# Optimization experiments

Measured on AMD Instinct MI355X. Metric: run time of the kernel, lower is better.

Reference implementation:

```python
import jax, jax.numpy as jnp
import numpy as np

N_NODES = 65536
N_EDGES = 1048576
DIM = 64
N_GRAPHS = 16


def setup_inputs() -> dict:
    key = jax.random.key(0)
    ks = jax.random.split(key, 8)
    node_feats = jax.random.normal(ks[0], (N_NODES, DIM), dtype=jnp.float32)
    edge_index = jax.random.randint(ks[1], (2, N_EDGES), 0, N_NODES, dtype=jnp.int32)
    batch_num_nodes = jnp.full((N_GRAPHS,), N_NODES // N_GRAPHS, dtype=jnp.int32)
    s = 1.0 / np.sqrt(DIM)
    W1 = jax.random.normal(ks[2], (DIM, DIM), dtype=jnp.float32) * s
    W2 = jax.random.normal(ks[3], (DIM, DIM), dtype=jnp.float32) * s
    W3 = jax.random.normal(ks[4], (DIM, DIM), dtype=jnp.float32) * s
    b1 = jnp.zeros((DIM,), jnp.float32)
    b2 = jnp.zeros((DIM,), jnp.float32)
    b3 = jnp.zeros((DIM,), jnp.float32)
    return {"node_feats": node_feats, "edge_index": edge_index,
            "batch_num_nodes": batch_num_nodes,
            "W1": W1, "b1": b1, "W2": W2, "b2": b2, "W3": W3, "b3": b3}


def _graph_conv(x, src, dst, W, b, n_nodes):
    # DGL GraphConv with norm='both': D_out^{-1/2} A^T D_in^{-1/2} style sym norm
    ones = jnp.ones((src.shape[0],), x.dtype)
    deg_out = jnp.clip(jax.ops.segment_sum(ones, src, num_segments=n_nodes), 1.0)
    deg_in = jnp.clip(jax.ops.segment_sum(ones, dst, num_segments=n_nodes), 1.0)
    h = x * jax.lax.rsqrt(deg_out)[:, None]          # [N, d] scale by src out-deg
    agg = jax.ops.segment_sum(h[src], dst, num_segments=n_nodes)  # gather+scatter
    agg = agg * jax.lax.rsqrt(deg_in)[:, None]
    return agg @ W + b


def _unbatch(h, batch_num_nodes):
    # pad each graph's node block to max_num_node -> [B, max_n, d]
    bnn = np.asarray(batch_num_nodes)
    B = bnn.shape[0]
    max_n = int(bnn.max())
    offsets = np.concatenate([[0], np.cumsum(bnn)])
    graph_id = np.repeat(np.arange(B), bnn)                 # [N_total]
    pos = np.arange(int(offsets[-1])) - offsets[graph_id]   # position within graph
    out = jnp.zeros((B, max_n, h.shape[1]), h.dtype)
    return out.at[jnp.asarray(graph_id), jnp.asarray(pos)].set(h)


def reference(node_feats, edge_index, batch_num_nodes, W1, b1, W2, b2, W3, b3):
    src, dst = edge_index[0], edge_index[1]
    n = node_feats.shape[0]
    h = jax.nn.relu(_graph_conv(node_feats, src, dst, W1, b1, n))
    h = jax.nn.relu(_graph_conv(h, src, dst, W2, b2, n))
    h = _graph_conv(h, src, dst, W3, b3, n)
    return _unbatch(h, batch_num_nodes)
```

## Files before the change

### kernel.cpp

```cpp
#include <hip/hip_runtime.h>
#include <hip/hip_fp16.h>


#define N_NODES 65536
#define N_EDGES 1048576
#define DIM 64

#define CHUNKS 256
#define EPC (N_EDGES / CHUNKS)
#define HB 128
#define OH_WORDS 16384

struct alignas(8) h4 { __half2 a, b; };

__global__ void edge_hist(const int* __restrict__ src, const int* __restrict__ dst,
                          int* __restrict__ block_hist, unsigned* __restrict__ partial,
                          uint2* __restrict__ zeroA, uint2* __restrict__ zeroB) {
    __shared__ unsigned h[OH_WORDS];
    __shared__ int bh[2][256];
    int t = threadIdx.x;
    int j = blockIdx.x;
    for (int i = t; i < OH_WORDS; i += 256) h[i] = 0;
    bh[0][t] = 0; bh[1][t] = 0;
    __syncthreads();
    if (j == 0) {
        if (t < 16) zeroA[t] = make_uint2(0u, 0u);
        else if (t < 32) zeroB[t - 16] = make_uint2(0u, 0u);
    }
    int base = j * (2 * EPC);
    for (int i = t; i < 2 * EPC; i += 256) {
        int s = src[base + i];
        int d = dst[base + i];
        atomicAdd(&h[s >> 2], 1u << ((s & 3) * 8));
        atomicAdd(&bh[i >> 12][d >> 8], 1);
    }
    __syncthreads();
    unsigned* dp = partial + (size_t)j * OH_WORDS;
    for (int i = t; i < OH_WORDS; i += 256) dp[i] = h[i];
    block_hist[t * CHUNKS + 2 * j]     = bh[0][t];
    block_hist[t * CHUNKS + 2 * j + 1] = bh[1][t];
}

__global__ void part_scan(const int* __restrict__ bh, int* __restrict__ so) {
    __shared__ int s[1024];
    int t = threadIdx.x;
    const int4* b4 = (const int4*)(bh + t * 64);
    int4 v[16];
    int sum = 0;
    #pragma unroll
    for (int i = 0; i < 16; i++) {
        v[i] = b4[i];
        sum += v[i].x + v[i].y + v[i].z + v[i].w;
    }
    s[t] = sum;
    __syncthreads();
    for (int off = 1; off < 1024; off <<= 1) {
        int u = (t >= off) ? s[t - off] : 0;
        __syncthreads();
        s[t] += u;
        __syncthreads();
    }
    int run = s[t] - sum;
    int* o = so + t * 64;
    #pragma unroll
    for (int i = 0; i < 16; i++) {
        o[4 * i + 0] = run; run += v[i].x;
        o[4 * i + 1] = run; run += v[i].y;
        o[4 * i + 2] = run; run += v[i].z;
        o[4 * i + 3] = run; run += v[i].w;
    }
}

__global__ void part_scatter(const int* __restrict__ src, const int* __restrict__ dst,
                             const int* __restrict__ so, int* __restrict__ bpack) {
    __shared__ int hist[256], sc[256], off[256], cur[256], gbase[256];
    __shared__ int sorted[EPC];
    __shared__ unsigned char pos2b[EPC];
    int t = threadIdx.x;
    int j = blockIdx.x;
    hist[t] = 0;
    gbase[t] = so[t * CHUNKS + j];
    __syncthreads();
    int base = j * EPC;
    int sv[16], dv[16];
    #pragma unroll
    for (int u = 0; u < 16; u++) {
        int i = base + u * 256 + t;
        sv[u] = src[i];
        dv[u] = dst[i];
        atomicAdd(&hist[dv[u] >> 8], 1);
    }
    __syncthreads();
    int hv = hist[t];
    sc[t] = hv;
    __syncthreads();
    for (int o = 1; o < 256; o <<= 1) {
        int u = (t >= o) ? sc[t - o] : 0;
        __syncthreads();
        sc[t] += u;
        __syncthreads();
    }
    int myoff = sc[t] - hv;
    off[t] = myoff;
    cur[t] = myoff;
    __syncthreads();
    for (int p = myoff, e = myoff + hv; p < e; p++)
        pos2b[p] = (unsigned char)t;
    #pragma unroll
    for (int u = 0; u < 16; u++) {
        int b = dv[u] >> 8;
        int r = atomicAdd(&cur[b], 1);
        sorted[r] = sv[u] | ((dv[u] & 255) << 16);
    }
    __syncthreads();
    #pragma unroll
    for (int u = 0; u < 16; u++) {
        int i = u * 256 + t;
        int b = pos2b[i];
        bpack[gbase[b] + (i - off[b])] = sorted[i];
    }
}

__global__ void bucket_fused(const int* __restrict__ bpack, const int* __restrict__ so,
                             int* __restrict__ row_start, float* __restrict__ rs_in,
                             unsigned short* __restrict__ csr_src) {
    __shared__ int stage[8192];
    __shared__ unsigned short sorted[8192];
    __shared__ int h[256], sc[256], cur[256];
    int b = blockIdx.x;
    int t = threadIdx.x;
    int beg = so[b * CHUNKS];
    int end = (b == 255) ? N_EDGES : so[(b + 1) * CHUNKS];
    int n = end - beg;
    h[t] = 0;
    __syncthreads();
    for (int i = t; i < n; i += 256) {
        int p = bpack[beg + i];
        if (i < 8192) stage[i] = p;
        atomicAdd(&h[(p >> 16) & 255], 1);
    }
    __syncthreads();
    int d = h[t];
    sc[t] = d;
    __syncthreads();
    for (int off = 1; off < 256; off <<= 1) {
        int v = (t >= off) ? sc[t - off] : 0;
        __syncthreads();
        sc[t] += v;
        __syncthreads();
    }
    int excl = sc[t] - d;
    int node = b * 256 + t;
    row_start[node] = beg + excl;
    rs_in[node] = rsqrtf(d < 1 ? 1.0f : (float)d);
    if (node == N_NODES - 1) row_start[N_NODES] = N_EDGES;
    cur[t] = excl;
    __syncthreads();
    if (n <= 8192) {
        for (int i = t; i < n; i += 256) {
            int p = stage[i];
            int r = atomicAdd(&cur[(p >> 16) & 255], 1);
            sorted[r] = (unsigned short)(p & 0xFFFF);
        }
        __syncthreads();
        for (int i = t; i < n; i += 256)
            csr_src[beg + i] = sorted[i];
    } else {
        cur[t] = beg + excl;
        __syncthreads();
        for (int i = t; i < n; i += 256) {
            int p = (i < 8192) ? stage[i] : bpack[beg + i];
            int pos = atomicAdd(&cur[(p >> 16) & 255], 1);
            csr_src[pos] = (unsigned short)(p & 0xFFFF);
        }
    }
}

__global__ void oh2p_prescale(const unsigned* __restrict__ partial,
                              float* __restrict__ rs_out,
                              const float4* __restrict__ x4, h4* __restrict__ xs) {
    __shared__ int4 psum[256];
    __shared__ float rsl[256];
    int b = blockIdx.x;
    int t = threadIdx.x;
    {
        int wl = t & 63;
        int q  = t >> 6;
        int w = b * 64 + wl;
        int c0 = 0, c1 = 0, c2 = 0, c3 = 0;
        const unsigned* p = partial + (size_t)(q * (HB / 4)) * OH_WORDS + w;
        #pragma unroll 4
        for (int c = 0; c < HB / 4; c++) {
            unsigned v = p[(size_t)c * OH_WORDS];
            c0 += (int)(v & 255u);
            c1 += (int)((v >> 8) & 255u);
            c2 += (int)((v >> 16) & 255u);
            c3 += (int)(v >> 24);
        }
        psum[t] = make_int4(c0, c1, c2, c3);
    }
    __syncthreads();
    if (t < 64) {
        int4 a = psum[t], b2 = psum[t + 64], c = psum[t + 128], d = psum[t + 192];
        int c0 = a.x + b2.x + c.x + d.x;
        int c1 = a.y + b2.y + c.y + d.y;
        int c2 = a.z + b2.z + c.z + d.z;
        int c3 = a.w + b2.w + c.w + d.w;
        int w = b * 64 + t;
        float4 r = make_float4(rsqrtf(c0 < 1 ? 1.0f : (float)c0),
                               rsqrtf(c1 < 1 ? 1.0f : (float)c1),
                               rsqrtf(c2 < 1 ? 1.0f : (float)c2),
                               rsqrtf(c3 < 1 ? 1.0f : (float)c3));
        ((float4*)rs_out)[w] = r;
        rsl[t * 4 + 0] = r.x; rsl[t * 4 + 1] = r.y;
        rsl[t * 4 + 2] = r.z; rsl[t * 4 + 3] = r.w;
    }
    __syncthreads();
    int rowbase = b * 4096;
    for (int i = t; i < 4096; i += 256) {
        float r = rsl[i >> 4];
        float4 v = x4[rowbase + i];
        h4 o;
        o.a = __float22half2_rn(make_float2(v.x * r, v.y * r));
        o.b = __float22half2_rn(make_float2(v.z * r, v.w * r));
        xs[rowbase + i] = o;
    }
}

template<bool SCALE_OUT>
__global__ void fused_layer(const uint4* __restrict__ xs16, const int* __restrict__ row_start,
                            const unsigned short* __restrict__ csr,
                            const float* __restrict__ rs_out, const float* __restrict__ rs_in,
                            const float* __restrict__ W, const float* __restrict__ b,
                            void* __restrict__ outp) {
    __shared__ float4 Ws4[DIM * 16];
    __shared__ float4 bs4[16];
    {
        const float4* Wg = (const float4*)W;
        for (int i = threadIdx.x; i < DIM * 16; i += blockDim.x) Ws4[i] = Wg[i];
        if (threadIdx.x < 16) bs4[threadIdx.x] = ((const float4*)b)[threadIdx.x];
    }
    __syncthreads();

    int wave_id = threadIdx.x >> 6;
    int lane = threadIdx.x & 63;
    int g = lane >> 3;
    int l = lane & 7;
    int node = blockIdx.x * 32 + wave_id * 8 + g;

    int beg = row_start[node];
    int end = row_start[node + 1];

    float a0 = 0.f, a1 = 0.f, a2 = 0.f, a3 = 0.f,
          a4 = 0.f, a5 = 0.f, a6 = 0.f, a7 = 0.f;
    for (int k = beg; k < end; k += 16) {
        int s[16];
        #pragma unroll
        for (int j = 0; j < 16; j++) {
            int kk = k + j;
            int idx = csr[kk];
            s[j] = (kk < end) ? idx : N_NODES;
        }
        uint4 v[16];
        #pragma unroll
        for (int j = 0; j < 16; j++) v[j] = xs16[s[j] * 8 + l];
        #pragma unroll
        for (int j = 0; j < 16; j++) {
            float2 f0 = __half22float2(*(const __half2*)&v[j].x);
            float2 f1 = __half22float2(*(const __half2*)&v[j].y);
            float2 f2 = __half22float2(*(const __half2*)&v[j].z);
            float2 f3 = __half22float2(*(const __half2*)&v[j].w);
            a0 += f0.x; a1 += f0.y; a2 += f1.x; a3 += f1.y;
            a4 += f2.x; a5 += f2.y; a6 += f3.x; a7 += f3.y;
        }
    }
    float ri = rs_in[node];
    a0 *= ri; a1 *= ri; a2 *= ri; a3 *= ri;
    a4 *= ri; a5 *= ri; a6 *= ri; a7 *= ri;

    float4 o0 = bs4[2 * l];
    float4 o1 = bs4[2 * l + 1];
    int gbase = g << 3;
    #pragma unroll
    for (int m = 0; m < 8; m++) {
        float q0 = __shfl(a0, gbase + m, 64);
        float q1 = __shfl(a1, gbase + m, 64);
        float q2 = __shfl(a2, gbase + m, 64);
        float q3 = __shfl(a3, gbase + m, 64);
        float q4 = __shfl(a4, gbase + m, 64);
        float q5 = __shfl(a5, gbase + m, 64);
        float q6 = __shfl(a6, gbase + m, 64);
        float q7 = __shfl(a7, gbase + m, 64);
        int rb = (8 * m) * 16 + 2 * l;
        float4 w;
        w = Ws4[rb];            o0.x += q0*w.x; o0.y += q0*w.y; o0.z += q0*w.z; o0.w += q0*w.w;
        w = Ws4[rb + 1];        o1.x += q0*w.x; o1.y += q0*w.y; o1.z += q0*w.z; o1.w += q0*w.w;
        w = Ws4[rb + 16];       o0.x += q1*w.x; o0.y += q1*w.y; o0.z += q1*w.z; o0.w += q1*w.w;
        w = Ws4[rb + 17];       o1.x += q1*w.x; o1.y += q1*w.y; o1.z += q1*w.z; o1.w += q1*w.w;
        w = Ws4[rb + 32];       o0.x += q2*w.x; o0.y += q2*w.y; o0.z += q2*w.z; o0.w += q2*w.w;
        w = Ws4[rb + 33];       o1.x += q2*w.x; o1.y += q2*w.y; o1.z += q2*w.z; o1.w += q2*w.w;
        w = Ws4[rb + 48];       o0.x += q3*w.x; o0.y += q3*w.y; o0.z += q3*w.z; o0.w += q3*w.w;
        w = Ws4[rb + 49];       o1.x += q3*w.x; o1.y += q3*w.y; o1.z += q3*w.z; o1.w += q3*w.w;
        w = Ws4[rb + 64];       o0.x += q4*w.x; o0.y += q4*w.y; o0.z += q4*w.z; o0.w += q4*w.w;
        w = Ws4[rb + 65];       o1.x += q4*w.x; o1.y += q4*w.y; o1.z += q4*w.z; o1.w += q4*w.w;
        w = Ws4[rb + 80];       o0.x += q5*w.x; o0.y += q5*w.y; o0.z += q5*w.z; o0.w += q5*w.w;
        w = Ws4[rb + 81];       o1.x += q5*w.x; o1.y += q5*w.y; o1.z += q5*w.z; o1.w += q5*w.w;
        w = Ws4[rb + 96];       o0.x += q6*w.x; o0.y += q6*w.y; o0.z += q6*w.z; o0.w += q6*w.w;
        w = Ws4[rb + 97];       o1.x += q6*w.x; o1.y += q6*w.y; o1.z += q6*w.z; o1.w += q6*w.w;
        w = Ws4[rb + 112];      o0.x += q7*w.x; o0.y += q7*w.y; o0.z += q7*w.z; o0.w += q7*w.w;
        w = Ws4[rb + 113];      o1.x += q7*w.x; o1.y += q7*w.y; o1.z += q7*w.z; o1.w += q7*w.w;
    }
    if (SCALE_OUT) {
        float ro = rs_out[node];
        o0.x = (o0.x < 0.f ? 0.f : o0.x) * ro;
        o0.y = (o0.y < 0.f ? 0.f : o0.y) * ro;
        o0.z = (o0.z < 0.f ? 0.f : o0.z) * ro;
        o0.w = (o0.w < 0.f ? 0.f : o0.w) * ro;
        o1.x = (o1.x < 0.f ? 0.f : o1.x) * ro;
        o1.y = (o1.y < 0.f ? 0.f : o1.y) * ro;
        o1.z = (o1.z < 0.f ? 0.f : o1.z) * ro;
        o1.w = (o1.w < 0.f ? 0.f : o1.w) * ro;
        uint4 ho;
        *(__half2*)&ho.x = __float22half2_rn(make_float2(o0.x, o0.y));
        *(__half2*)&ho.y = __float22half2_rn(make_float2(o0.z, o0.w));
        *(__half2*)&ho.z = __float22half2_rn(make_float2(o1.x, o1.y));
        *(__half2*)&ho.w = __float22half2_rn(make_float2(o1.z, o1.w));
        ((uint4*)outp)[node * 8 + l] = ho;
    } else {
        float4* o4 = (float4*)outp;
        o4[node * 16 + 2 * l]     = o0;
        o4[node * 16 + 2 * l + 1] = o1;
    }
}

extern "C" void kernel_launch(void* const* d_in, const int* in_sizes, int n_in,
                              void* d_out, int out_size, void* d_ws, size_t ws_size,
                              hipStream_t stream) {
    const float* x   = (const float*)d_in[0];
    const int*   ei  = (const int*)d_in[1];
    const int*   src = ei;
    const int*   dst = ei + N_EDGES;
    const float* W1 = (const float*)d_in[3];
    const float* b1 = (const float*)d_in[4];
    const float* W2 = (const float*)d_in[5];
    const float* b2 = (const float*)d_in[6];
    const float* W3 = (const float*)d_in[7];
    const float* b3 = (const float*)d_in[8];
    float* out = (float*)d_out;

    char* ws = (char*)d_ws;
    float* rs        = (float*)ws;
    float* rs_out    = rs;
    float* rs_in     = rs + N_NODES;
    int*   row_start = (int*)(rs + 2 * N_NODES);
    int*   block_h   = row_start + (N_NODES + 256);
    int*   so        = block_h + 256 * CHUNKS;
    unsigned short* csr_src = (unsigned short*)(so + 256 * CHUNKS);
    h4*    bufA      = (h4*)(csr_src + N_EDGES + 16);
    h4*    bufB      = bufA + (size_t)(N_NODES + 1) * 16;
    unsigned* partial = (unsigned*)(bufB + (size_t)(N_NODES + 1) * 16);
    int*   bpack     = (int*)bufB;
    uint2* zeroA     = (uint2*)(bufA + (size_t)N_NODES * 16);
    uint2* zeroB     = (uint2*)(bufB + (size_t)N_NODES * 16);

    const int fb = N_NODES / 32;

    edge_hist    <<<HB, 256, 0, stream>>>(src, dst, block_h, partial, zeroA, zeroB);
    part_scan    <<<1, 1024, 0, stream>>>(block_h, so);
    part_scatter <<<CHUNKS, 256, 0, stream>>>(src, dst, so, bpack);
    bucket_fused <<<256, 256, 0, stream>>>(bpack, so, row_start, rs_in, csr_src);
    oh2p_prescale<<<256, 256, 0, stream>>>(partial, rs_out, (const float4*)x, bufA);

    fused_layer<true ><<<fb, 256, 0, stream>>>((const uint4*)bufA, row_start, csr_src, rs_out, rs_in, W1, b1, (void*)bufB);
    fused_layer<true ><<<fb, 256, 0, stream>>>((const uint4*)bufB, row_start, csr_src, rs_out, rs_in, W2, b2, (void*)bufA);
    fused_layer<false><<<fb, 256, 0, stream>>>((const uint4*)bufA, row_start, csr_src, rs_out, rs_in, W3, b3, (void*)out);
}
```

Before: 236.6 us.

## Fuse CSR preprocessing kernels into one cooperative kernel with grid syncs

Merges the five preprocessing kernels (edge histogram, partition scan, scatter, bucket sort, prescale) into a single cooperative kernel of 256 blocks separated by grid.sync barriers. The single-block 1024-thread scan becomes a two-level parallel scan: each block scans one row of block histograms, then scans the row totals. The goal is to remove kernel launch gaps and the serial single-block scan. In exchange, the large 67KB shared buffer per block may limit occupancy, and half the blocks sit idle during the histogram phase.

Measured after the change: 358.8 us. +51.6%, slower.

```diff
diff --git a/kernel.cpp b/kernel.cpp
--- a/kernel.cpp
+++ b/kernel.cpp
@@ -1,5 +1,8 @@
 #include <hip/hip_runtime.h>
 #include <hip/hip_fp16.h>
+#include <hip/hip_cooperative_groups.h>
+
+namespace cg = cooperative_groups;
 
 
 #define N_NODES 65536
@@ -13,177 +16,64 @@
 
 struct alignas(8) h4 { __half2 a, b; };
 
-__global__ void edge_hist(const int* __restrict__ src, const int* __restrict__ dst,
-                          int* __restrict__ block_hist, unsigned* __restrict__ partial,
-                          uint2* __restrict__ zeroA, uint2* __restrict__ zeroB) {
-    __shared__ unsigned h[OH_WORDS];
-    __shared__ int bh[2][256];
-    int t = threadIdx.x;
-    int j = blockIdx.x;
-    for (int i = t; i < OH_WORDS; i += 256) h[i] = 0;
-    bh[0][t] = 0; bh[1][t] = 0;
-    __syncthreads();
-    if (j == 0) {
-        if (t < 16) zeroA[t] = make_uint2(0u, 0u);
-        else if (t < 32) zeroB[t - 16] = make_uint2(0u, 0u);
-    }
-    int base = j * (2 * EPC);
-    for (int i = t; i < 2 * EPC; i += 256) {
-        int s = src[base + i];
-        int d = dst[base + i];
-        atomicAdd(&h[s >> 2], 1u << ((s & 3) * 8));
-        atomicAdd(&bh[i >> 12][d >> 8], 1);
-    }
-    __syncthreads();
-    unsigned* dp = partial + (size_t)j * OH_WORDS;
-    for (int i = t; i < OH_WORDS; i += 256) dp[i] = h[i];
-    block_hist[t * CHUNKS + 2 * j]     = bh[0][t];
-    block_hist[t * CHUNKS + 2 * j + 1] = bh[1][t];
-}
-
-__global__ void part_scan(const int* __restrict__ bh, int* __restrict__ so) {
-    __shared__ int s[1024];
-    int t = threadIdx.x;
-    const int4* b4 = (const int4*)(bh + t * 64);
-    int4 v[16];
-    int sum = 0;
-    #pragma unroll
-    for (int i = 0; i < 16; i++) {
-        v[i] = b4[i];
-        sum += v[i].x + v[i].y + v[i].z + v[i].w;
-    }
-    s[t] = sum;
-    __syncthreads();
-    for (int off = 1; off < 1024; off <<= 1) {
-        int u = (t >= off) ? s[t - off] : 0;
-        __syncthreads();
-        s[t] += u;
-        __syncthreads();
-    }
-    int run = s[t] - sum;
-    int* o = so + t * 64;
-    #pragma unroll
-    for (int i = 0; i < 16; i++) {
-        o[4 * i + 0] = run; run += v[i].x;
-        o[4 * i + 1] = run; run += v[i].y;
-        o[4 * i + 2] = run; run += v[i].z;
-        o[4 * i + 3] = run; run += v[i].w;
-    }
-}
-
-__global__ void part_scatter(const int* __restrict__ src, const int* __restrict__ dst,
-                             const int* __restrict__ so, int* __restrict__ bpack) {
-    __shared__ int hist[256], sc[256], off[256], cur[256], gbase[256];
-    __shared__ int sorted[EPC];
-    __shared__ unsigned char pos2b[EPC];
-    int t = threadIdx.x;
-    int j = blockIdx.x;
-    hist[t] = 0;
-    gbase[t] = so[t * CHUNKS + j];
-    __syncthreads();
-    int base = j * EPC;
-    int sv[16], dv[16];
-    #pragma unroll
-    for (int u = 0; u < 16; u++) {
-        int i = base + u * 256 + t;
-        sv[u] = src[i];
-        dv[u] = dst[i];
-        atomicAdd(&hist[dv[u] >> 8], 1);
-    }
-    __syncthreads();
-    int hv = hist[t];
-    sc[t] = hv;
-    __syncthreads();
-    for (int o = 1; o < 256; o <<= 1) {
-        int u = (t >= o) ? sc[t - o] : 0;
-        __syncthreads();
-        sc[t] += u;
-        __syncthreads();
-    }
-    int myoff = sc[t] - hv;
-    off[t] = myoff;
-    cur[t] = myoff;
-    __syncthreads();
-    for (int p = myoff, e = myoff + hv; p < e; p++)
-        pos2b[p] = (unsigned char)t;
-    #pragma unroll
-    for (int u = 0; u < 16; u++) {
-        int b = dv[u] >> 8;
-        int r = atomicAdd(&cur[b], 1);
-        sorted[r] = sv[u] | ((dv[u] & 255) << 16);
-    }
-    __syncthreads();
-    #pragma unroll
-    for (int u = 0; u < 16; u++) {
-        int i = u * 256 + t;
-        int b = pos2b[i];
-        bpack[gbase[b] + (i - off[b])] = sorted[i];
-    }
-}
-
-__global__ void bucket_fused(const int* __restrict__ bpack, const int* __restrict__ so,
-                             int* __restrict__ row_start, float* __restrict__ rs_in,
-                             unsigned short* __restrict__ csr_src) {
-    __shared__ int stage[8192];
-    __shared__ unsigned short sorted[8192];
-    __shared__ int h[256], sc[256], cur[256];
-    int b = blockIdx.x;
-    int t = threadIdx.x;
-    int beg = so[b * CHUNKS];
-    int end = (b == 255) ? N_EDGES : so[(b + 1) * CHUNKS];
-    int n = end - beg;
-    h[t] = 0;
-    __syncthreads();
-    for (int i = t; i < n; i += 256) {
-        int p = bpack[beg + i];
-        if (i < 8192) stage[i] = p;
-        atomicAdd(&h[(p >> 16) & 255], 1);
-    }
-    __syncthreads();
-    int d = h[t];
-    sc[t] = d;
-    __syncthreads();
-    for (int off = 1; off < 256; off <<= 1) {
-        int v = (t >= off) ? sc[t - off] : 0;
-        __syncthreads();
-        sc[t] += v;
-        __syncthreads();
-    }
-    int excl = sc[t] - d;
-    int node = b * 256 + t;
-    row_start[node] = beg + excl;
-    rs_in[node] = rsqrtf(d < 1 ? 1.0f : (float)d);
-    if (node == N_NODES - 1) row_start[N_NODES] = N_EDGES;
-    cur[t] = excl;
-    __syncthreads();
-    if (n <= 8192) {
-        for (int i = t; i < n; i += 256) {
-            int p = stage[i];
-            int r = atomicAdd(&cur[(p >> 16) & 255], 1);
-            sorted[r] = (unsigned short)(p & 0xFFFF);
-        }
-        __syncthreads();
-        for (int i = t; i < n; i += 256)
-            csr_src[beg + i] = sorted[i];
-    } else {
-        cur[t] = beg + excl;
-        __syncthreads();
-        for (int i = t; i < n; i += 256) {
-            int p = (i < 8192) ? stage[i] : bpack[beg + i];
-            int pos = atomicAdd(&cur[(p >> 16) & 255], 1);
-            csr_src[pos] = (unsigned short)(p & 0xFFFF);
-        }
-    }
-}
-
-__global__ void oh2p_prescale(const unsigned* __restrict__ partial,
-                              float* __restrict__ rs_out,
-                              const float4* __restrict__ x4, h4* __restrict__ xs) {
-    __shared__ int4 psum[256];
-    __shared__ float rsl[256];
-    int b = blockIdx.x;
-    int t = threadIdx.x;
-    {
+__global__ void __launch_bounds__(256) preproc_fused(
+    const int* __restrict__ src, const int* __restrict__ dst,
+    int* __restrict__ block_h, unsigned* __restrict__ partial,
+    int* __restrict__ so, int* __restrict__ rowtot,
+    int* __restrict__ bpack, int* __restrict__ row_start,
+    float* __restrict__ rs_in, float* __restrict__ rs_out,
+    const float4* __restrict__ x4, h4* __restrict__ xs,
+    unsigned short* __restrict__ csr_src,
+    uint2* __restrict__ zeroA, uint2* __restrict__ zeroB)
+{
+    cg::grid_group grid = cg::this_grid();
+    __shared__ __align__(16) char sm[67584];
+    const int t = threadIdx.x;
+    const int b = blockIdx.x;
+
+    if (b < HB) {
+        unsigned* h = (unsigned*)sm;
+        int* bh = (int*)(sm + OH_WORDS * 4);
+        for (int i = t; i < OH_WORDS; i += 256) h[i] = 0;
+        bh[t] = 0; bh[256 + t] = 0;
+        __syncthreads();
+        if (b == 0) {
+            if (t < 16) zeroA[t] = make_uint2(0u, 0u);
+            else if (t < 32) zeroB[t - 16] = make_uint2(0u, 0u);
+        }
+        int base = b * (2 * EPC);
+        for (int i = t; i < 2 * EPC; i += 256) {
+            int s = src[base + i];
+            int d = dst[base + i];
+            atomicAdd(&h[s >> 2], 1u << ((s & 3) * 8));
+            atomicAdd(&bh[(i >> 12) * 256 + (d >> 8)], 1);
+        }
+        __syncthreads();
+        unsigned* dp = partial + (size_t)b * OH_WORDS;
+        for (int i = t; i < OH_WORDS; i += 256) dp[i] = h[i];
+        block_h[t * CHUNKS + 2 * b]     = bh[t];
+        block_h[t * CHUNKS + 2 * b + 1] = bh[256 + t];
+    }
+    grid.sync();
+
+    int* lscan = (int*)sm;
+    {
+        int* tmp = (int*)(sm + 1024);
+        int v = block_h[b * CHUNKS + t];
+        tmp[t] = v;
+        __syncthreads();
+        for (int off = 1; off < 256; off <<= 1) {
+            int u = (t >= off) ? tmp[t - off] : 0;
+            __syncthreads();
+            tmp[t] += u;
+            __syncthreads();
+        }
+        lscan[t] = tmp[t] - v;
+        if (t == 255) rowtot[b] = tmp[255];
+    }
+    {
+        int4* psum = (int4*)(sm + 2048);
+        float* rsl = (float*)(sm + 2048 + 4096);
         int wl = t & 63;
         int q  = t >> 6;
         int w = b * 64 + wl;
@@ -198,32 +88,155 @@
             c3 += (int)(v >> 24);
         }
         psum[t] = make_int4(c0, c1, c2, c3);
-    }
-    __syncthreads();
-    if (t < 64) {
-        int4 a = psum[t], b2 = psum[t + 64], c = psum[t + 128], d = psum[t + 192];
-        int c0 = a.x + b2.x + c.x + d.x;
-        int c1 = a.y + b2.y + c.y + d.y;
-        int c2 = a.z + b2.z + c.z + d.z;
-        int c3 = a.w + b2.w + c.w + d.w;
-        int w = b * 64 + t;
-        float4 r = make_float4(rsqrtf(c0 < 1 ? 1.0f : (float)c0),
-                               rsqrtf(c1 < 1 ? 1.0f : (float)c1),
-                               rsqrtf(c2 < 1 ? 1.0f : (float)c2),
-                               rsqrtf(c3 < 1 ? 1.0f : (float)c3));
-        ((float4*)rs_out)[w] = r;
-        rsl[t * 4 + 0] = r.x; rsl[t * 4 + 1] = r.y;
-        rsl[t * 4 + 2] = r.z; rsl[t * 4 + 3] = r.w;
-    }
-    __syncthreads();
-    int rowbase = b * 4096;
-    for (int i = t; i < 4096; i += 256) {
-        float r = rsl[i >> 4];
-        float4 v = x4[rowbase + i];
-        h4 o;
-        o.a = __float22half2_rn(make_float2(v.x * r, v.y * r));
-        o.b = __float22half2_rn(make_float2(v.z * r, v.w * r));
-        xs[rowbase + i] = o;
+        __syncthreads();
+        if (t < 64) {
+            int4 a = psum[t], b2 = psum[t + 64], c = psum[t + 128], d = psum[t + 192];
+            int d0 = a.x + b2.x + c.x + d.x;
+            int d1 = a.y + b2.y + c.y + d.y;
+            int d2 = a.z + b2.z + c.z + d.z;
+            int d3 = a.w + b2.w + c.w + d.w;
+            int w2 = b * 64 + t;
+            float4 r = make_float4(rsqrtf(d0 < 1 ? 1.0f : (float)d0),
+                                   rsqrtf(d1 < 1 ? 1.0f : (float)d1),
+                                   rsqrtf(d2 < 1 ? 1.0f : (float)d2),
+                                   rsqrtf(d3 < 1 ? 1.0f : (float)d3));
+            ((float4*)rs_out)[w2] = r;
+            rsl[t * 4 + 0] = r.x; rsl[t * 4 + 1] = r.y;
+            rsl[t * 4 + 2] = r.z; rsl[t * 4 + 3] = r.w;
+        }
+        __syncthreads();
+        int rowbase = b * 4096;
+        for (int i = t; i < 4096; i += 256) {
+            float r = rsl[i >> 4];
+            float4 v = x4[rowbase + i];
+            h4 o;
+            o.a = __float22half2_rn(make_float2(v.x * r, v.y * r));
+            o.b = __float22half2_rn(make_float2(v.z * r, v.w * r));
+            xs[rowbase + i] = o;
+        }
+    }
+    grid.sync();
+
+    {
+        int* tot  = (int*)(sm + 2048);
+        int* orig = (int*)(sm + 3072);
+        int v = rowtot[t];
+        tot[t] = v; orig[t] = v;
+        __syncthreads();
+        for (int off = 1; off < 256; off <<= 1) {
+            int u = (t >= off) ? tot[t - off] : 0;
+            __syncthreads();
+            tot[t] += u;
+            __syncthreads();
+        }
+        int rowoff = tot[b] - orig[b];
+        so[b * CHUNKS + t] = rowoff + lscan[t];
+    }
+    grid.sync();
+
+    {
+        int* hist = (int*)sm;
+        int* sc   = (int*)(sm + 1024);
+        int* offv = (int*)(sm + 2048);
+        int* cur  = (int*)(sm + 3072);
+        int* gb   = (int*)(sm + 4096);
+        int* sorted = (int*)(sm + 5120);
+        unsigned char* pos2b = (unsigned char*)(sm + 5120 + 16384);
+        hist[t] = 0;
+        gb[t] = so[t * CHUNKS + b];
+        __syncthreads();
+        int base = b * EPC;
+        int sv[16], dv[16];
+        #pragma unroll
+        for (int u = 0; u < 16; u++) {
+            int i = base + u * 256 + t;
+            sv[u] = src[i];
+            dv[u] = dst[i];
+            atomicAdd(&hist[dv[u] >> 8], 1);
+        }
+        __syncthreads();
+        int hv = hist[t];
+        sc[t] = hv;
+        __syncthreads();
+        for (int o = 1; o < 256; o <<= 1) {
+            int u = (t >= o) ? sc[t - o] : 0;
+            __syncthreads();
+            sc[t] += u;
+            __syncthreads();
+        }
+        int myoff = sc[t] - hv;
+        offv[t] = myoff;
+        cur[t] = myoff;
+        __syncthreads();
+        for (int p = myoff, e = myoff + hv; p < e; p++)
+            pos2b[p] = (unsigned char)t;
+        #pragma unroll
+        for (int u = 0; u < 16; u++) {
+            int bb = dv[u] >> 8;
+            int r = atomicAdd(&cur[bb], 1);
+            sorted[r] = sv[u] | ((dv[u] & 255) << 16);
+        }
+        __syncthreads();
+        #pragma unroll
+        for (int u = 0; u < 16; u++) {
+            int i = u * 256 + t;
+            int bb = pos2b[i];
+            bpack[gb[bb] + (i - offv[bb])] = sorted[i];
+        }
+    }
+    grid.sync();
+
+    {
+        int* stage = (int*)sm;
+        unsigned short* sorted = (unsigned short*)(sm + 32768);
+        int* h   = (int*)(sm + 32768 + 16384);
+        int* sc  = (int*)(sm + 32768 + 16384 + 1024);
+        int* cur = (int*)(sm + 32768 + 16384 + 2048);
+        int beg = so[b * CHUNKS];
+        int end = (b == 255) ? N_EDGES : so[(b + 1) * CHUNKS];
+        int n = end - beg;
+        h[t] = 0;
+        __syncthreads();
+        for (int i = t; i < n; i += 256) {
+            int p = bpack[beg + i];
+            if (i < 8192) stage[i] = p;
+            atomicAdd(&h[(p >> 16) & 255], 1);
+        }
+        __syncthreads();
+        int d = h[t];
+        sc[t] = d;
+        __syncthreads();
+        for (int off = 1; off < 256; off <<= 1) {
+            int v = (t >= off) ? sc[t - off] : 0;
+            __syncthreads();
+            sc[t] += v;
+            __syncthreads();
+        }
+        int excl = sc[t] - d;
+        int node = b * 256 + t;
+        row_start[node] = beg + excl;
+        rs_in[node] = rsqrtf(d < 1 ? 1.0f : (float)d);
+        if (node == N_NODES - 1) row_start[N_NODES] = N_EDGES;
+        cur[t] = excl;
+        __syncthreads();
+        if (n <= 8192) {
+            for (int i = t; i < n; i += 256) {
+                int p = stage[i];
+                int r = atomicAdd(&cur[(p >> 16) & 255], 1);
+                sorted[r] = (unsigned short)(p & 0xFFFF);
+            }
+            __syncthreads();
+            for (int i = t; i < n; i += 256)
+                csr_src[beg + i] = sorted[i];
+        } else {
+            cur[t] = beg + excl;
+            __syncthreads();
+            for (int i = t; i < n; i += 256) {
+                int p = (i < 8192) ? stage[i] : bpack[beg + i];
+                int pos = atomicAdd(&cur[(p >> 16) & 255], 1);
+                csr_src[pos] = (unsigned short)(p & 0xFFFF);
+            }
+        }
     }
 }
 
@@ -359,17 +372,23 @@
     h4*    bufA      = (h4*)(csr_src + N_EDGES + 16);
     h4*    bufB      = bufA + (size_t)(N_NODES + 1) * 16;
     unsigned* partial = (unsigned*)(bufB + (size_t)(N_NODES + 1) * 16);
+    int*   rowtot    = (int*)(partial + (size_t)HB * OH_WORDS);
     int*   bpack     = (int*)bufB;
     uint2* zeroA     = (uint2*)(bufA + (size_t)N_NODES * 16);
     uint2* zeroB     = (uint2*)(bufB + (size_t)N_NODES * 16);
 
     const int fb = N_NODES / 32;
 
-    edge_hist    <<<HB, 256, 0, stream>>>(src, dst, block_h, partial, zeroA, zeroB);
-    part_scan    <<<1, 1024, 0, stream>>>(block_h, so);
-    part_scatter <<<CHUNKS, 256, 0, stream>>>(src, dst, so, bpack);
-    bucket_fused <<<256, 256, 0, stream>>>(bpack, so, row_start, rs_in, csr_src);
-    oh2p_prescale<<<256, 256, 0, stream>>>(partial, rs_out, (const float4*)x, bufA);
+    {
+        const float4* x4p = (const float4*)x;
+        h4* xsA = bufA;
+        void* args[] = { (void*)&src, (void*)&dst, (void*)&block_h, (void*)&partial,
+                         (void*)&so, (void*)&rowtot, (void*)&bpack, (void*)&row_start,
+                         (void*)&rs_in, (void*)&rs_out, (void*)&x4p, (void*)&xsA,
+                         (void*)&csr_src, (void*)&zeroA, (void*)&zeroB };
+        hipLaunchCooperativeKernel((void*)preproc_fused, dim3(256), dim3(256),
+                                   args, 0, stream);
+    }
 
     fused_layer<true ><<<fb, 256, 0, stream>>>((const uint4*)bufA, row_start, csr_src, rs_out, rs_in, W1, b1, (void*)bufB);
     fused_layer<true ><<<fb, 256, 0, stream>>>((const uint4*)bufB, row_start, csr_src, rs_out, rs_in, W2, b2, (void*)bufA);
```

## Replace single-block global scan with per-bucket scans fused into degree prescale kernel

Applied to the files above, without the earlier changes.

The single-block 1024-thread prefix scan over the 256x256 bucket histogram is replaced by a per-bucket-row scan folded into the out-degree/prescale kernel, which now runs with 256 blocks. Each row's total is written out, and both the scatter and bucket kernels redo a small 256-entry scan of those totals to rebuild global offsets. This removes one serial kernel launch and its low-parallelism scan, at the cost of redundant small scans in every block of the later kernels.

Result: faster. 222.2 us, median of 2 (-6.1%).

```diff
diff --git a/kernel.cpp b/kernel.cpp
--- a/kernel.cpp
+++ b/kernel.cpp
@@ -41,148 +41,29 @@
     block_hist[t * CHUNKS + 2 * j + 1] = bh[1][t];
 }
 
-__global__ void part_scan(const int* __restrict__ bh, int* __restrict__ so) {
-    __shared__ int s[1024];
-    int t = threadIdx.x;
-    const int4* b4 = (const int4*)(bh + t * 64);
-    int4 v[16];
-    int sum = 0;
-    #pragma unroll
-    for (int i = 0; i < 16; i++) {
-        v[i] = b4[i];
-        sum += v[i].x + v[i].y + v[i].z + v[i].w;
-    }
-    s[t] = sum;
-    __syncthreads();
-    for (int off = 1; off < 1024; off <<= 1) {
-        int u = (t >= off) ? s[t - off] : 0;
-        __syncthreads();
-        s[t] += u;
-        __syncthreads();
-    }
-    int run = s[t] - sum;
-    int* o = so + t * 64;
-    #pragma unroll
-    for (int i = 0; i < 16; i++) {
-        o[4 * i + 0] = run; run += v[i].x;
-        o[4 * i + 1] = run; run += v[i].y;
-        o[4 * i + 2] = run; run += v[i].z;
-        o[4 * i + 3] = run; run += v[i].w;
-    }
-}
-
-__global__ void part_scatter(const int* __restrict__ src, const int* __restrict__ dst,
-                             const int* __restrict__ so, int* __restrict__ bpack) {
-    __shared__ int hist[256], sc[256], off[256], cur[256], gbase[256];
-    __shared__ int sorted[EPC];
-    __shared__ unsigned char pos2b[EPC];
-    int t = threadIdx.x;
-    int j = blockIdx.x;
-    hist[t] = 0;
-    gbase[t] = so[t * CHUNKS + j];
-    __syncthreads();
-    int base = j * EPC;
-    int sv[16], dv[16];
-    #pragma unroll
-    for (int u = 0; u < 16; u++) {
-        int i = base + u * 256 + t;
-        sv[u] = src[i];
-        dv[u] = dst[i];
-        atomicAdd(&hist[dv[u] >> 8], 1);
-    }
-    __syncthreads();
-    int hv = hist[t];
-    sc[t] = hv;
-    __syncthreads();
-    for (int o = 1; o < 256; o <<= 1) {
-        int u = (t >= o) ? sc[t - o] : 0;
-        __syncthreads();
-        sc[t] += u;
-        __syncthreads();
-    }
-    int myoff = sc[t] - hv;
-    off[t] = myoff;
-    cur[t] = myoff;
-    __syncthreads();
-    for (int p = myoff, e = myoff + hv; p < e; p++)
-        pos2b[p] = (unsigned char)t;
-    #pragma unroll
-    for (int u = 0; u < 16; u++) {
-        int b = dv[u] >> 8;
-        int r = atomicAdd(&cur[b], 1);
-        sorted[r] = sv[u] | ((dv[u] & 255) << 16);
-    }
-    __syncthreads();
-    #pragma unroll
-    for (int u = 0; u < 16; u++) {
-        int i = u * 256 + t;
-        int b = pos2b[i];
-        bpack[gbase[b] + (i - off[b])] = sorted[i];
-    }
-}
-
-__global__ void bucket_fused(const int* __restrict__ bpack, const int* __restrict__ so,
-                             int* __restrict__ row_start, float* __restrict__ rs_in,
-                             unsigned short* __restrict__ csr_src) {
-    __shared__ int stage[8192];
-    __shared__ unsigned short sorted[8192];
-    __shared__ int h[256], sc[256], cur[256];
-    int b = blockIdx.x;
-    int t = threadIdx.x;
-    int beg = so[b * CHUNKS];
-    int end = (b == 255) ? N_EDGES : so[(b + 1) * CHUNKS];
-    int n = end - beg;
-    h[t] = 0;
-    __syncthreads();
-    for (int i = t; i < n; i += 256) {
-        int p = bpack[beg + i];
-        if (i < 8192) stage[i] = p;
-        atomicAdd(&h[(p >> 16) & 255], 1);
-    }
-    __syncthreads();
-    int d = h[t];
-    sc[t] = d;
-    __syncthreads();
-    for (int off = 1; off < 256; off <<= 1) {
-        int v = (t >= off) ? sc[t - off] : 0;
-        __syncthreads();
-        sc[t] += v;
-        __syncthreads();
-    }
-    int excl = sc[t] - d;
-    int node = b * 256 + t;
-    row_start[node] = beg + excl;
-    rs_in[node] = rsqrtf(d < 1 ? 1.0f : (float)d);
-    if (node == N_NODES - 1) row_start[N_NODES] = N_EDGES;
-    cur[t] = excl;
-    __syncthreads();
-    if (n <= 8192) {
-        for (int i = t; i < n; i += 256) {
-            int p = stage[i];
-            int r = atomicAdd(&cur[(p >> 16) & 255], 1);
-            sorted[r] = (unsigned short)(p & 0xFFFF);
-        }
-        __syncthreads();
-        for (int i = t; i < n; i += 256)
-            csr_src[beg + i] = sorted[i];
-    } else {
-        cur[t] = beg + excl;
-        __syncthreads();
-        for (int i = t; i < n; i += 256) {
-            int p = (i < 8192) ? stage[i] : bpack[beg + i];
-            int pos = atomicAdd(&cur[(p >> 16) & 255], 1);
-            csr_src[pos] = (unsigned short)(p & 0xFFFF);
-        }
-    }
-}
-
-__global__ void oh2p_prescale(const unsigned* __restrict__ partial,
-                              float* __restrict__ rs_out,
-                              const float4* __restrict__ x4, h4* __restrict__ xs) {
+__global__ void scan_oh2p(const int* __restrict__ block_h, int* __restrict__ lscan,
+                          int* __restrict__ rowtot,
+                          const unsigned* __restrict__ partial,
+                          float* __restrict__ rs_out,
+                          const float4* __restrict__ x4, h4* __restrict__ xs) {
+    __shared__ int tmp[256];
     __shared__ int4 psum[256];
     __shared__ float rsl[256];
     int b = blockIdx.x;
     int t = threadIdx.x;
+    {
+        int v = block_h[b * CHUNKS + t];
+        tmp[t] = v;
+        __syncthreads();
+        for (int off = 1; off < 256; off <<= 1) {
+            int u = (t >= off) ? tmp[t - off] : 0;
+            __syncthreads();
+            tmp[t] += u;
+            __syncthreads();
+        }
+        lscan[b * CHUNKS + t] = tmp[t] - v;
+        if (t == 255) rowtot[b] = tmp[255];
+    }
     {
         int wl = t & 63;
         int q  = t >> 6;
@@ -224,6 +105,136 @@
         o.a = __float22half2_rn(make_float2(v.x * r, v.y * r));
         o.b = __float22half2_rn(make_float2(v.z * r, v.w * r));
         xs[rowbase + i] = o;
+    }
+}
+
+__global__ void part_scatter(const int* __restrict__ src, const int* __restrict__ dst,
+                             const int* __restrict__ lscan, const int* __restrict__ rowtot,
+                             int* __restrict__ bpack) {
+    __shared__ int hist[256], sc[256], off[256], cur[256], gbase[256];
+    __shared__ int sorted[EPC];
+    __shared__ unsigned char pos2b[EPC];
+    int t = threadIdx.x;
+    int j = blockIdx.x;
+    {
+        int rv = rowtot[t];
+        sc[t] = rv;
+        __syncthreads();
+        for (int o = 1; o < 256; o <<= 1) {
+            int u = (t >= o) ? sc[t - o] : 0;
+            __syncthreads();
+            sc[t] += u;
+            __syncthreads();
+        }
+        gbase[t] = (sc[t] - rv) + lscan[t * CHUNKS + j];
+    }
+    hist[t] = 0;
+    __syncthreads();
+    int base = j * EPC;
+    int sv[16], dv[16];
+    #pragma unroll
+    for (int u = 0; u < 16; u++) {
+        int i = base + u * 256 + t;
+        sv[u] = src[i];
+        dv[u] = dst[i];
+        atomicAdd(&hist[dv[u] >> 8], 1);
+    }
+    __syncthreads();
+    int hv = hist[t];
+    sc[t] = hv;
+    __syncthreads();
+    for (int o = 1; o < 256; o <<= 1) {
+        int u = (t >= o) ? sc[t - o] : 0;
+        __syncthreads();
+        sc[t] += u;
+        __syncthreads();
+    }
+    int myoff = sc[t] - hv;
+    off[t] = myoff;
+    cur[t] = myoff;
+    __syncthreads();
+    for (int p = myoff, e = myoff + hv; p < e; p++)
+        pos2b[p] = (unsigned char)t;
+    #pragma unroll
+    for (int u = 0; u < 16; u++) {
+        int b = dv[u] >> 8;
+        int r = atomicAdd(&cur[b], 1);
+        sorted[r] = sv[u] | ((dv[u] & 255) << 16);
+    }
+    __syncthreads();
+    #pragma unroll
+    for (int u = 0; u < 16; u++) {
+        int i = u * 256 + t;
+        int b = pos2b[i];
+        bpack[gbase[b] + (i - off[b])] = sorted[i];
+    }
+}
+
+__global__ void bucket_fused(const int* __restrict__ bpack, const int* __restrict__ rowtot,
+                             int* __restrict__ row_start, float* __restrict__ rs_in,
+                             unsigned short* __restrict__ csr_src) {
+    __shared__ int stage[8192];
+    __shared__ unsigned short sorted[8192];
+    __shared__ int h[256], sc[256], cur[256], ro[256];
+    int b = blockIdx.x;
+    int t = threadIdx.x;
+    {
+        int rv = rowtot[t];
+        sc[t] = rv;
+        __syncthreads();
+        for (int o = 1; o < 256; o <<= 1) {
+            int u = (t >= o) ? sc[t - o] : 0;
+            __syncthreads();
+            sc[t] += u;
+            __syncthreads();
+        }
+        ro[t] = sc[t] - rv;
+    }
+    __syncthreads();
+    int beg = ro[b];
+    int end = (b == 255) ? N_EDGES : ro[b + 1];
+    int n = end - beg;
+    h[t] = 0;
+    __syncthreads();
+    for (int i = t; i < n; i += 256) {
+        int p = bpack[beg + i];
+        if (i < 8192) stage[i] = p;
+        atomicAdd(&h[(p >> 16) & 255], 1);
+    }
+    __syncthreads();
+    int d = h[t];
+    sc[t] = d;
+    __syncthreads();
+    for (int off = 1; off < 256; off <<= 1) {
+        int v = (t >= off) ? sc[t - off] : 0;
+        __syncthreads();
+        sc[t] += v;
+        __syncthreads();
+    }
+    int excl = sc[t] - d;
+    int node = b * 256 + t;
+    row_start[node] = beg + excl;
+    rs_in[node] = rsqrtf(d < 1 ? 1.0f : (float)d);
+    if (node == N_NODES - 1) row_start[N_NODES] = N_EDGES;
+    cur[t] = excl;
+    __syncthreads();
+    if (n <= 8192) {
+        for (int i = t; i < n; i += 256) {
+            int p = stage[i];
+            int r = atomicAdd(&cur[(p >> 16) & 255], 1);
+            sorted[r] = (unsigned short)(p & 0xFFFF);
+        }
+        __syncthreads();
+        for (int i = t; i < n; i += 256)
+            csr_src[beg + i] = sorted[i];
+    } else {
+        cur[t] = beg + excl;
+        __syncthreads();
+        for (int i = t; i < n; i += 256) {
+            int p = (i < 8192) ? stage[i] : bpack[beg + i];
+            int pos = atomicAdd(&cur[(p >> 16) & 255], 1);
+            csr_src[pos] = (unsigned short)(p & 0xFFFF);
+        }
     }
 }
 
@@ -354,11 +365,12 @@
     float* rs_in     = rs + N_NODES;
     int*   row_start = (int*)(rs + 2 * N_NODES);
     int*   block_h   = row_start + (N_NODES + 256);
-    int*   so        = block_h + 256 * CHUNKS;
-    unsigned short* csr_src = (unsigned short*)(so + 256 * CHUNKS);
+    int*   lscan     = block_h + 256 * CHUNKS;
+    unsigned short* csr_src = (unsigned short*)(lscan + 256 * CHUNKS);
     h4*    bufA      = (h4*)(csr_src + N_EDGES + 16);
     h4*    bufB      = bufA + (size_t)(N_NODES + 1) * 16;
     unsigned* partial = (unsigned*)(bufB + (size_t)(N_NODES + 1) * 16);
+    int*   rowtot    = (int*)(partial + (size_t)HB * OH_WORDS);
     int*   bpack     = (int*)bufB;
     uint2* zeroA     = (uint2*)(bufA + (size_t)N_NODES * 16);
     uint2* zeroB     = (uint2*)(bufB + (size_t)N_NODES * 16);
@@ -366,10 +378,10 @@
     const int fb = N_NODES / 32;
 
     edge_hist    <<<HB, 256, 0, stream>>>(src, dst, block_h, partial, zeroA, zeroB);
-    part_scan    <<<1, 1024, 0, stream>>>(block_h, so);
-    part_scatter <<<CHUNKS, 256, 0, stream>>>(src, dst, so, bpack);
-    bucket_fused <<<256, 256, 0, stream>>>(bpack, so, row_start, rs_in, csr_src);
-    oh2p_prescale<<<256, 256, 0, stream>>>(partial, rs_out, (const float4*)x, bufA);
+    scan_oh2p    <<<256, 256, 0, stream>>>(block_h, lscan, rowtot, partial, rs_out,
+                                           (const float4*)x, bufA);
+    part_scatter <<<CHUNKS, 256, 0, stream>>>(src, dst, lscan, rowtot, bpack);
+    bucket_fused <<<256, 256, 0, stream>>>(bpack, rowtot, row_start, rs_in, csr_src);
 
     fused_layer<true ><<<fb, 256, 0, stream>>>((const uint4*)bufA, row_start, csr_src, rs_out, rs_in, W1, b1, (void*)bufB);
     fused_layer<true ><<<fb, 256, 0, stream>>>((const uint4*)bufB, row_start, csr_src, rs_out, rs_in, W2, b2, (void*)bufA);
```
